# Performance work log

Measured on AMD Instinct MI355X. Metric: run time of the kernel, lower is better.

Reference implementation:

```python
import jax, jax.numpy as jnp
import numpy as np

B, T = 8, 1024
C_IN, C_H = 4096, 4096
K_I, K_H = 3, 3
INIT_SPARSITY = 0.15


def _fixed_fanin_bipartite(rng, n_out, n_in, k):
    # exactly k True entries per row, distinct columns
    r = rng.random((n_out, n_in))
    cols = np.argsort(r, axis=1)[:, :k]
    A = np.zeros((n_out, n_in), np.float32)
    np.put_along_axis(A, cols, 1.0, axis=1)
    return A


def _fixed_fanin_graph(rng, n, k):
    # exactly k True entries per row, distinct non-self columns
    r = rng.random((n, n))
    np.fill_diagonal(r, 2.0)  # exclude self-loops
    cols = np.argsort(r, axis=1)[:, :k]
    A = np.zeros((n, n), np.float32)
    np.put_along_axis(A, cols, 1.0, axis=1)
    return A


def setup_inputs() -> dict:
    rng = np.random.default_rng(0)
    z = jnp.asarray(rng.random((B, T, C_IN)) < INIT_SPARSITY)          # bool (B,T,C_in)
    h0 = jnp.asarray(rng.random((B, C_H)) < INIT_SPARSITY)             # bool (B,C_h)
    A_input_f = jnp.asarray(_fixed_fanin_bipartite(rng, C_H, C_IN, K_I))  # (C_h,C_in) f32
    A_hidden_f = jnp.asarray(_fixed_fanin_graph(rng, C_H, K_H))           # (C_h,C_h) f32
    return {"z": z, "h0": h0, "A_input_f": A_input_f, "A_hidden_f": A_hidden_f}


def reference(z, h0, A_input_f, A_hidden_f):
    # AND-of-ORs CA: h_i(t) = [OR over input fan-in of z(t)] AND [OR over hidden fan-in of h(t-1)]
    z_tf = jnp.moveaxis(z, -2, 0)  # (T, B, C_in)

    def step(h, z_t):
        input_or = (z_t.astype(jnp.float32) @ A_input_f.T) > 0   # (B, C_h) bool
        hidden_or = (h.astype(jnp.float32) @ A_hidden_f.T) > 0   # (B, C_h) bool
        h_new = input_or & hidden_or
        return h_new, h_new

    _, h_seq = jax.lax.scan(step, h0, z_tf)   # (T, B, C_h)
    h_seq = jnp.moveaxis(h_seq, 0, -2)        # (B, T, C_h)
    return jnp.concatenate([z, h_seq], axis=-1)  # (B, T, C_in + C_h) bool
```

## Files before the change

### kernel.cpp

```cpp
#include <hip/hip_runtime.h>
#include <stdint.h>

#define B_   8
#define T_   1024
#define CIN_ 4096
#define CH_  4096


__device__ __forceinline__ uint32_t bytes_nonzero01(uint32_t w) {
  uint32_t t = (w & 0x7F7F7F7Fu) + 0x7F7F7F7Fu;
  t = (t | w) & 0x80808080u;
  return t >> 7;
}

__device__ __forceinline__ uint32_t load4(const void* base, long idx4, int es) {
  if (es == 1) {
    uint32_t w = ((const uint32_t*)base)[idx4];
    return bytes_nonzero01(w);
  } else if (es == 2) {
    uint32_t w0 = ((const uint32_t*)base)[idx4 * 2];
    uint32_t w1 = ((const uint32_t*)base)[idx4 * 2 + 1];
    uint32_t r = 0;
    r |= ((w0 & 0xFFFFu) != 0u) ? 0x00000001u : 0u;
    r |= ((w0 >> 16)     != 0u) ? 0x00000100u : 0u;
    r |= ((w1 & 0xFFFFu) != 0u) ? 0x00010000u : 0u;
    r |= ((w1 >> 16)     != 0u) ? 0x01000000u : 0u;
    return r;
  } else {
    uint4 w = ((const uint4*)base)[idx4];
    uint32_t r = 0;
    r |= (w.x != 0u) ? 0x00000001u : 0u;
    r |= (w.y != 0u) ? 0x00000100u : 0u;
    r |= (w.z != 0u) ? 0x00010000u : 0u;
    r |= (w.w != 0u) ? 0x01000000u : 0u;
    return r;
  }
}

__device__ __forceinline__ uint4 expand01(uint32_t v4) {
  uint4 r = { v4 & 1u, (v4 >> 8) & 1u, (v4 >> 16) & 1u, (v4 >> 24) & 1u };
  return r;
}

__global__ __launch_bounds__(256) void extract_kernel(const float* __restrict__ Ain,
                                                      const float* __restrict__ Ah,
                                                      uint32_t* __restrict__ idxin,
                                                      uint32_t* __restrict__ idxh,
                                                      const uint32_t* __restrict__ z,
                                                      uint32_t* __restrict__ modep) {
  if (blockIdx.x == 2048) {
    __shared__ int sB, sH, sW, sL;
    const int n = threadIdx.x;
    if (n == 0) { sB = 1; sH = 1; sW = 1; sL = 0; }
    __syncthreads();
    int okB = 1, okH = 1, okW = 1, low = 0;
    for (int k = 0; k < 16; ++k) {
      uint32_t w = z[n + 256 * k];
      if ((w & 0xFEFEFEFEu) != 0u) okB = 0;
      uint32_t lo = w & 0xFFFFu, hi = w >> 16;
      if (!((lo == 0u || lo == 0x3F80u) && (hi == 0u || hi == 0x3F80u))) okH = 0;
      if (!(w == 0u || w == 1u)) okW = 0;
      if (lo != 0u) low = 1;
    }
    if (!okB) atomicAnd(&sB, 0);
    if (!okH) atomicAnd(&sH, 0);
    if (!okW) atomicAnd(&sW, 0);
    if (low)  atomicOr(&sL, 1);
    __syncthreads();
    if (n == 0) {
      uint32_t mode;
      if (sW)      mode = 4;
      else if (sB) mode = 1;
      else if (sH) mode = sL ? 2 : 4;
      else         mode = 1;
      modep[0] = mode;
    }
    return;
  }
  const int wave = threadIdx.x >> 6;
  const int lane = threadIdx.x & 63;
  const int row  = blockIdx.x * 4 + wave;
  const float* A;
  uint32_t* outp;
  if (row < 4096) { A = Ain + (long)row * 4096;          outp = idxin + row * 3; }
  else            { A = Ah  + (long)(row - 4096) * 4096; outp = idxh + (row - 4096) * 3; }
  __shared__ int cnt[4];
  if (lane == 0) cnt[wave] = 0;
  __syncthreads();
  const float4* A4 = (const float4*)A;
  #pragma unroll
  for (int it = 0; it < 16; ++it) {
    float4 v = A4[it * 64 + lane];
    int cbase = (it * 64 + lane) * 4;
    if (v.x != 0.0f) { int p = atomicAdd(&cnt[wave], 1); if (p < 3) outp[p] = cbase;     }
    if (v.y != 0.0f) { int p = atomicAdd(&cnt[wave], 1); if (p < 3) outp[p] = cbase + 1; }
    if (v.z != 0.0f) { int p = atomicAdd(&cnt[wave], 1); if (p < 3) outp[p] = cbase + 2; }
    if (v.w != 0.0f) { int p = atomicAdd(&cnt[wave], 1); if (p < 3) outp[p] = cbase + 3; }
  }
}

__global__ __launch_bounds__(1024) void inor_kernel(const void* __restrict__ z,
                                                    const uint32_t* __restrict__ idxin,
                                                    const uint32_t* __restrict__ modep,
                                                    uint32_t* __restrict__ in_orb,
                                                    uint32_t* __restrict__ out) {
  const int t = blockIdx.x;
  const int n = threadIdx.x;
  const int es = (int)modep[0];
  __shared__ __align__(16) unsigned char zp[4096];
  uint32_t acc = 0;
  #pragma unroll
  for (int b = 0; b < B_; ++b) {
    uint32_t v4 = load4(z, ((long)b * T_ + t) * 1024 + n, es);
    acc |= v4 << b;
    ((uint4*)(out + ((long)b * T_ + t) * 8192))[n] = expand01(v4);
  }
  ((uint32_t*)zp)[n] = acc;
  __syncthreads();
  const uint4* ip = (const uint4*)(idxin + n * 12);
  uint4 q0 = ip[0], q1 = ip[1], q2 = ip[2];
  uint32_t r0 = (uint32_t)zp[q0.x] | zp[q0.y] | zp[q0.z];
  uint32_t r1 = (uint32_t)zp[q0.w] | zp[q1.x] | zp[q1.y];
  uint32_t r2 = (uint32_t)zp[q1.z] | zp[q1.w] | zp[q2.x];
  uint32_t r3 = (uint32_t)zp[q2.y] | zp[q2.z] | zp[q2.w];
  in_orb[t * 1024 + n] = r0 | (r1 << 8) | (r2 << 16) | (r3 << 24);
}

__global__ __launch_bounds__(1024) void scan_kernel(const uint32_t* __restrict__ in_orb,
                                                    const uint32_t* __restrict__ idxh,
                                                    const void* __restrict__ h0,
                                                    const uint32_t* __restrict__ modep,
                                                    uint32_t* __restrict__ out) {
  const int b = blockIdx.x;
  const int n = threadIdx.x;
  const int es = (int)modep[0];
  __shared__ __align__(16) unsigned char hbuf[2][4096];

  uint32_t d[4][3];
  {
    const uint4* p = (const uint4*)(idxh + n * 12);
    uint4 q0 = p[0], q1 = p[1], q2 = p[2];
    d[0][0] = q0.x; d[0][1] = q0.y; d[0][2] = q0.z;
    d[1][0] = q0.w; d[1][1] = q1.x; d[1][2] = q1.y;
    d[2][0] = q1.z; d[2][1] = q1.w; d[2][2] = q2.x;
    d[3][0] = q2.y; d[3][1] = q2.z; d[3][2] = q2.w;
  }

  ((uint32_t*)hbuf[0])[n] = load4(h0, (long)b * 1024 + n, es);
  __syncthreads();

  uint32_t* outh = out + (long)b * T_ * 8192 + 4096;

  int p = 0;
  uint32_t inw = in_orb[n];
  for (int t = 0; t < T_; ++t) {
    uint32_t inw_next = (t + 1 < T_) ? in_orb[(t + 1) * 1024 + n] : 0u;
    const unsigned char* hc = &hbuf[p][0];
    unsigned char* hn = &hbuf[p ^ 1][0];

    uint32_t mask = (inw >> b) & 0x01010101u;
    uint32_t out4 = 0;
    if (mask) {
      if (mask & 0x00000001u) {
        uint32_t v = (uint32_t)hc[d[0][0]] | hc[d[0][1]] | hc[d[0][2]];
        out4 |= v;
      }
      if (mask & 0x00000100u) {
        uint32_t v = (uint32_t)hc[d[1][0]] | hc[d[1][1]] | hc[d[1][2]];
        out4 |= v << 8;
      }
      if (mask & 0x00010000u) {
        uint32_t v = (uint32_t)hc[d[2][0]] | hc[d[2][1]] | hc[d[2][2]];
        out4 |= v << 16;
      }
      if (mask & 0x01000000u) {
        uint32_t v = (uint32_t)hc[d[3][0]] | hc[d[3][1]] | hc[d[3][2]];
        out4 |= v << 24;
      }
    }
    ((uint32_t*)hn)[n] = out4;
    ((uint4*)(outh + (long)t * 8192))[n] = expand01(out4);
    __syncthreads();

    inw = inw_next;
    p ^= 1;
  }
}

extern "C" void kernel_launch(void* const* d_in, const int* in_sizes, int n_in,
                              void* d_out, int out_size, void* d_ws, size_t ws_size,
                              hipStream_t stream) {
  const void*  z   = d_in[0];
  const void*  h0  = d_in[1];
  const float* Ain = (const float*)d_in[2];
  const float* Ah  = (const float*)d_in[3];
  uint32_t* out = (uint32_t*)d_out;

  char* ws = (char*)d_ws;
  uint32_t* modep = (uint32_t*)(ws);
  uint32_t* idxin = (uint32_t*)(ws + 256);
  uint32_t* idxh  = (uint32_t*)(ws + 256 + 49152);
  uint32_t* inorb = (uint32_t*)(ws + 98560);

  extract_kernel<<<2049, 256,  0, stream>>>(Ain, Ah, idxin, idxh,
                                            (const uint32_t*)z, modep);
  inor_kernel   <<<T_,   1024, 0, stream>>>(z, idxin, modep, inorb, out);
  scan_kernel   <<<B_,   1024, 0, stream>>>(inorb, idxh, h0, modep, out);
}
```

Baseline: 951.9 us.

## Overlap z-to-output copy with serial scan and batch in_orb staging

Moves the expansion of z into the output out of inor_kernel and into extra blocks of the scan kernel, so the bulk copy runs concurrently with the 8-block serial scan instead of before it. The scan now stages 16 timesteps of in_orb into shared memory per group and defers its output stores until after each group of 16 steps, taking global loads and stores off the per-step critical path. It also raises the scan blocks' wave priority. The 88KB shared allocation applies to every block, including the copy blocks, which may limit how many copy blocks run at once.

```diff
diff --git a/kernel.cpp b/kernel.cpp
--- a/kernel.cpp
+++ b/kernel.cpp
@@ -5,6 +5,9 @@
 #define T_   1024
 #define CIN_ 4096
 #define CH_  4096
+#define GRP  16
+#define NGRP (T_ / GRP)
+#define NCOPY 512
 
 
 __device__ __forceinline__ uint32_t bytes_nonzero01(uint32_t w) {
@@ -92,29 +95,25 @@
   for (int it = 0; it < 16; ++it) {
     float4 v = A4[it * 64 + lane];
     int cbase = (it * 64 + lane) * 4;
-    if (v.x != 0.0f) { int p = atomicAdd(&cnt[wave], 1); if (p < 3) outp[p] = cbase;     }
-    if (v.y != 0.0f) { int p = atomicAdd(&cnt[wave], 1); if (p < 3) outp[p] = cbase + 1; }
-    if (v.z != 0.0f) { int p = atomicAdd(&cnt[wave], 1); if (p < 3) outp[p] = cbase + 2; }
-    if (v.w != 0.0f) { int p = atomicAdd(&cnt[wave], 1); if (p < 3) outp[p] = cbase + 3; }
+    if (v.x != 0.0f) { int q = atomicAdd(&cnt[wave], 1); if (q < 3) outp[q] = cbase;     }
+    if (v.y != 0.0f) { int q = atomicAdd(&cnt[wave], 1); if (q < 3) outp[q] = cbase + 1; }
+    if (v.z != 0.0f) { int q = atomicAdd(&cnt[wave], 1); if (q < 3) outp[q] = cbase + 2; }
+    if (v.w != 0.0f) { int q = atomicAdd(&cnt[wave], 1); if (q < 3) outp[q] = cbase + 3; }
   }
 }
 
 __global__ __launch_bounds__(1024) void inor_kernel(const void* __restrict__ z,
                                                     const uint32_t* __restrict__ idxin,
                                                     const uint32_t* __restrict__ modep,
-                                                    uint32_t* __restrict__ in_orb,
-                                                    uint32_t* __restrict__ out) {
+                                                    uint32_t* __restrict__ in_orb) {
   const int t = blockIdx.x;
   const int n = threadIdx.x;
   const int es = (int)modep[0];
   __shared__ __align__(16) unsigned char zp[4096];
   uint32_t acc = 0;
   #pragma unroll
-  for (int b = 0; b < B_; ++b) {
-    uint32_t v4 = load4(z, ((long)b * T_ + t) * 1024 + n, es);
-    acc |= v4 << b;
-    ((uint4*)(out + ((long)b * T_ + t) * 8192))[n] = expand01(v4);
-  }
+  for (int b = 0; b < B_; ++b)
+    acc |= load4(z, ((long)b * T_ + t) * 1024 + n, es) << b;
   ((uint32_t*)zp)[n] = acc;
   __syncthreads();
   const uint4* ip = (const uint4*)(idxin + n * 12);
@@ -126,15 +125,33 @@
   in_orb[t * 1024 + n] = r0 | (r1 << 8) | (r2 << 16) | (r3 << 24);
 }
 
-__global__ __launch_bounds__(1024) void scan_kernel(const uint32_t* __restrict__ in_orb,
-                                                    const uint32_t* __restrict__ idxh,
-                                                    const void* __restrict__ h0,
-                                                    const uint32_t* __restrict__ modep,
-                                                    uint32_t* __restrict__ out) {
-  const int b = blockIdx.x;
+__global__ __launch_bounds__(1024) void scan_copy_kernel(const uint32_t* __restrict__ in_orb,
+                                                         const uint32_t* __restrict__ idxh,
+                                                         const void* __restrict__ h0,
+                                                         const void* __restrict__ z,
+                                                         const uint32_t* __restrict__ modep,
+                                                         uint32_t* __restrict__ out) {
   const int n = threadIdx.x;
   const int es = (int)modep[0];
-  __shared__ __align__(16) unsigned char hbuf[2][4096];
+
+  if (blockIdx.x >= 8) {
+    const long total4 = (long)B_ * T_ * 1024;
+    const long stride = (long)NCOPY * 1024;
+    uint4* out4 = (uint4*)out;
+    for (long i4 = (long)(blockIdx.x - 8) * 1024 + n; i4 < total4; i4 += stride) {
+      uint32_t v = load4(z, i4, es);
+      long row = i4 >> 10, c4 = i4 & 1023;
+      out4[row * 2048 + c4] = expand01(v);
+    }
+    return;
+  }
+
+  __builtin_amdgcn_s_setprio(1);
+  __shared__ __align__(16) unsigned char smem[88 * 1024];
+  unsigned char* hb0 = &smem[0];
+  unsigned char* hb1 = &smem[4096];
+  uint32_t* stg = (uint32_t*)&smem[8192];
+  const int b = blockIdx.x;
 
   uint32_t d[4][3];
   {
@@ -145,45 +162,40 @@
     d[2][0] = q1.z; d[2][1] = q1.w; d[2][2] = q2.x;
     d[3][0] = q2.y; d[3][1] = q2.z; d[3][2] = q2.w;
   }
-
-  ((uint32_t*)hbuf[0])[n] = load4(h0, (long)b * 1024 + n, es);
-  __syncthreads();
-
+  ((uint32_t*)hb0)[n] = load4(h0, (long)b * 1024 + n, es);
   uint32_t* outh = out + (long)b * T_ * 8192 + 4096;
 
-  int p = 0;
-  uint32_t inw = in_orb[n];
-  for (int t = 0; t < T_; ++t) {
-    uint32_t inw_next = (t + 1 < T_) ? in_orb[(t + 1) * 1024 + n] : 0u;
-    const unsigned char* hc = &hbuf[p][0];
-    unsigned char* hn = &hbuf[p ^ 1][0];
-
-    uint32_t mask = (inw >> b) & 0x01010101u;
-    uint32_t out4 = 0;
-    if (mask) {
-      if (mask & 0x00000001u) {
-        uint32_t v = (uint32_t)hc[d[0][0]] | hc[d[0][1]] | hc[d[0][2]];
-        out4 |= v;
+  for (int g = 0; g < NGRP; ++g) {
+    {
+      const uint4* src = (const uint4*)(in_orb + g * (GRP * 1024));
+      uint4 s0 = src[n], s1 = src[n + 1024], s2 = src[n + 2048], s3 = src[n + 3072];
+      uint4* dst = (uint4*)stg;
+      dst[n] = s0; dst[n + 1024] = s1; dst[n + 2048] = s2; dst[n + 3072] = s3;
+    }
+    __syncthreads();
+
+    uint32_t oacc[GRP];
+    #pragma unroll
+    for (int tt = 0; tt < GRP; ++tt) {
+      const unsigned char* hc = (tt & 1) ? hb1 : hb0;
+      unsigned char* hn = (tt & 1) ? hb0 : hb1;
+      uint32_t inw = stg[tt * 1024 + n];
+      uint32_t mask = (inw >> b) & 0x01010101u;
+      uint32_t o4 = 0;
+      if (mask) {
+        if (mask & 0x00000001u) { uint32_t v = (uint32_t)hc[d[0][0]] | hc[d[0][1]] | hc[d[0][2]]; o4 |= v; }
+        if (mask & 0x00000100u) { uint32_t v = (uint32_t)hc[d[1][0]] | hc[d[1][1]] | hc[d[1][2]]; o4 |= v << 8; }
+        if (mask & 0x00010000u) { uint32_t v = (uint32_t)hc[d[2][0]] | hc[d[2][1]] | hc[d[2][2]]; o4 |= v << 16; }
+        if (mask & 0x01000000u) { uint32_t v = (uint32_t)hc[d[3][0]] | hc[d[3][1]] | hc[d[3][2]]; o4 |= v << 24; }
       }
-      if (mask & 0x00000100u) {
-        uint32_t v = (uint32_t)hc[d[1][0]] | hc[d[1][1]] | hc[d[1][2]];
-        out4 |= v << 8;
-      }
-      if (mask & 0x00010000u) {
-        uint32_t v = (uint32_t)hc[d[2][0]] | hc[d[2][1]] | hc[d[2][2]];
-        out4 |= v << 16;
-      }
-      if (mask & 0x01000000u) {
-        uint32_t v = (uint32_t)hc[d[3][0]] | hc[d[3][1]] | hc[d[3][2]];
-        out4 |= v << 24;
-      }
-    }
-    ((uint32_t*)hn)[n] = out4;
-    ((uint4*)(outh + (long)t * 8192))[n] = expand01(out4);
-    __syncthreads();
-
-    inw = inw_next;
-    p ^= 1;
+      ((uint32_t*)hn)[n] = o4;
+      oacc[tt] = o4;
+      __syncthreads();
+    }
+
+    #pragma unroll
+    for (int tt = 0; tt < GRP; ++tt)
+      ((uint4*)(outh + (long)(g * GRP + tt) * 8192))[n] = expand01(oacc[tt]);
   }
 }
 
@@ -202,8 +214,8 @@
   uint32_t* idxh  = (uint32_t*)(ws + 256 + 49152);
   uint32_t* inorb = (uint32_t*)(ws + 98560);
 
-  extract_kernel<<<2049, 256,  0, stream>>>(Ain, Ah, idxin, idxh,
-                                            (const uint32_t*)z, modep);
-  inor_kernel   <<<T_,   1024, 0, stream>>>(z, idxin, modep, inorb, out);
-  scan_kernel   <<<B_,   1024, 0, stream>>>(inorb, idxh, h0, modep, out);
-}
+  extract_kernel  <<<2049, 256,  0, stream>>>(Ain, Ah, idxin, idxh,
+                                              (const uint32_t*)z, modep);
+  inor_kernel     <<<T_,   1024, 0, stream>>>(z, idxin, modep, inorb);
+  scan_copy_kernel<<<8 + NCOPY, 1024, 0, stream>>>(inorb, idxh, h0, z, modep, out);
+}
```

New measurement: 1.173 ms. 1.23x slower.
